# Optimization experiments

Measured on AMD Instinct MI355X. Metric: run time of the kernel, lower is better.

Reference implementation:

```python
import jax, jax.numpy as jnp
import numpy as np
from jax import lax

C = 16        # class_nums
START = 14    # tag_to_idx['<START>']
STOP = 15     # tag_to_idx['<STOP>']
NEG = -10000.0
B, T, V, E, H = 64, 512, 50000, 512, 1024
HD = H // 2   # per-direction hidden size


def setup_inputs() -> dict:
    key = jax.random.key(0)
    ks = jax.random.split(key, 16)
    s = 0.05
    inp = {}
    inp["sentence"] = jax.random.randint(ks[0], (B, T), 0, V)
    inp["embedding"] = jax.random.normal(ks[1], (V, E), jnp.float32) * 0.1
    # LSTM params, torch layout: [4*HD, Din] with gate order i,f,g,o; leading dim 2 = (fwd, bwd)
    inp["w_ih_l0"] = jax.random.normal(ks[2], (2, 4 * HD, E), jnp.float32) * s
    inp["w_hh_l0"] = jax.random.normal(ks[3], (2, 4 * HD, HD), jnp.float32) * s
    inp["b_ih_l0"] = jax.random.normal(ks[4], (2, 4 * HD), jnp.float32) * s
    inp["b_hh_l0"] = jax.random.normal(ks[5], (2, 4 * HD), jnp.float32) * s
    inp["w_ih_l1"] = jax.random.normal(ks[6], (2, 4 * HD, H), jnp.float32) * s
    inp["w_hh_l1"] = jax.random.normal(ks[7], (2, 4 * HD, HD), jnp.float32) * s
    inp["b_ih_l1"] = jax.random.normal(ks[8], (2, 4 * HD), jnp.float32) * s
    inp["b_hh_l1"] = jax.random.normal(ks[9], (2, 4 * HD), jnp.float32) * s
    inp["lin_w"] = jax.random.normal(ks[10], (C, H), jnp.float32) * s
    inp["lin_b"] = jax.random.normal(ks[11], (C,), jnp.float32) * s
    tr = jax.random.normal(ks[12], (C, C), jnp.float32)
    inp["transitions"] = tr.at[START, :].set(NEG).at[:, STOP].set(NEG)
    # init_hidden(): random (h0, c0), shape [2*num_layers, B, HD]
    inp["h0"] = jax.random.normal(ks[13], (4, B, HD), jnp.float32)
    inp["c0"] = jax.random.normal(ks[14], (4, B, HD), jnp.float32)
    return inp


def _lstm_dir(x, w_ih, w_hh, b_ih, b_hh, h0, c0, reverse):
    # x: [T, B, Din] -> hs: [T, B, HD]
    def step(carry, xt):
        h, c = carry
        g = xt @ w_ih.T + h @ w_hh.T + b_ih + b_hh  # [B, 4*HD]
        i, f, gc, o = jnp.split(g, 4, axis=-1)       # torch gate order: i, f, g, o
        c = jax.nn.sigmoid(f) * c + jax.nn.sigmoid(i) * jnp.tanh(gc)
        h = jax.nn.sigmoid(o) * jnp.tanh(c)
        return (h, c), h
    _, hs = lax.scan(step, (h0, c0), x, reverse=reverse)
    return hs


def _features(sentence, embedding, w_ih_l0, w_hh_l0, b_ih_l0, b_hh_l0,
              w_ih_l1, w_hh_l1, b_ih_l1, b_hh_l1, lin_w, lin_b, h0, c0):
    x = embedding[sentence].transpose(1, 0, 2)  # [T, B, E]
    # layer 0 (bidirectional)
    hf = _lstm_dir(x, w_ih_l0[0], w_hh_l0[0], b_ih_l0[0], b_hh_l0[0], h0[0], c0[0], False)
    hb = _lstm_dir(x, w_ih_l0[1], w_hh_l0[1], b_ih_l0[1], b_hh_l0[1], h0[1], c0[1], True)
    x = jnp.concatenate([hf, hb], axis=-1)      # [T, B, H]
    # layer 1 (bidirectional)
    hf = _lstm_dir(x, w_ih_l1[0], w_hh_l1[0], b_ih_l1[0], b_hh_l1[0], h0[2], c0[2], False)
    hb = _lstm_dir(x, w_ih_l1[1], w_hh_l1[1], b_ih_l1[1], b_hh_l1[1], h0[3], c0[3], True)
    x = jnp.concatenate([hf, hb], axis=-1)      # [T, B, H]
    feats = x @ lin_w.T + lin_b                 # [T, B, C]
    return feats.transpose(1, 0, 2)             # [B, T, C]


def _viterbi(feats, transitions):
    # feats: [T, C]. Vectorized over the tag dim; scan over time.
    init = jnp.full((C,), NEG, feats.dtype).at[START].set(0.0)

    def step(fv, feat_t):
        scores = fv[None, :] + transitions      # [next_tag, prev_tag]
        bp = jnp.argmax(scores, axis=1)
        return jnp.max(scores, axis=1) + feat_t, bp

    fv, bps = lax.scan(step, init, feats)       # bps: [T, C]
    terminal = fv + transitions[STOP]
    best = jnp.argmax(terminal)

    def back(tag, bp_t):
        return bp_t[tag], tag

    _, path = lax.scan(back, best, bps, reverse=True)  # [T]
    return terminal[best], path


def reference(sentence, embedding, w_ih_l0, w_hh_l0, b_ih_l0, b_hh_l0,
              w_ih_l1, w_hh_l1, b_ih_l1, b_hh_l1, lin_w, lin_b,
              transitions, h0, c0):
    feats = _features(sentence, embedding, w_ih_l0, w_hh_l0, b_ih_l0, b_hh_l0,
                      w_ih_l1, w_hh_l1, b_ih_l1, b_hh_l1, lin_w, lin_b, h0, c0)
    scores, paths = jax.vmap(_viterbi, in_axes=(0, None))(feats, transitions)
    return scores, paths
```

## Files before the change

### kernel.cpp

```cpp
#include <hip/hip_runtime.h>
#include <stdint.h>

constexpr int kB  = 64;
constexpr int kT  = 512;
constexpr int kHD = 512;
constexpr int kC  = 16;
constexpr int kL  = 32;
constexpr int kSTART = 14;
constexpr int kSTOP  = 15;
#define NEGV (-10000.0f)

typedef __bf16 bf16x8 __attribute__((ext_vector_type(8)));
typedef float  f32x4  __attribute__((ext_vector_type(4)));

union U16x8 { uint4 u; bf16x8 v; };

__device__ __forceinline__ unsigned short f2bf(float f) {
    union { float f; unsigned int u; } x; x.f = f;
    unsigned int u = x.u;
    u += 0x7fffu + ((u >> 16) & 1u);
    return (unsigned short)(u >> 16);
}
__device__ __forceinline__ float bf2f(unsigned int hbits) {
    union { unsigned int u; float f; } x; x.u = hbits << 16;
    return x.f;
}
__device__ __forceinline__ float fsig(float x) {
    return __builtin_amdgcn_rcpf(1.f + __expf(-x));
}
__device__ __forceinline__ float ftanh(float x) {
    float e = __expf(2.f * x);
    return 1.f - 2.f * __builtin_amdgcn_rcpf(e + 1.f);
}

typedef __attribute__((address_space(1))) const unsigned int GASU;
typedef __attribute__((address_space(3))) unsigned int LASU;
__device__ __forceinline__ void ld_lds16(const unsigned short* g, unsigned short* l) {
    __builtin_amdgcn_global_load_lds((GASU*)g, (LASU*)l, 16, 0, 0);
}

__global__ void k_castWx(const float* __restrict__ src, unsigned short* __restrict__ dst, int K) {
    int np = blockIdx.x;
    int dd = np >> 11, r = np & 2047;
    int g = r & 3, cj = r >> 2;
    const float* s = src + ((size_t)(dd * 2048 + g * 512 + cj)) * K;
    unsigned short* d = dst + (size_t)np * K;
    for (int e = threadIdx.x * 8; e < K; e += 128 * 8) {
        float4 a = *(const float4*)(s + e);
        float4 b = *(const float4*)(s + e + 4);
        ushort4 lo, hi;
        lo.x = f2bf(a.x); lo.y = f2bf(a.y); lo.z = f2bf(a.z); lo.w = f2bf(a.w);
        hi.x = f2bf(b.x); hi.y = f2bf(b.y); hi.z = f2bf(b.z); hi.w = f2bf(b.w);
        *(ushort4*)(d + e) = lo; *(ushort4*)(d + e + 4) = hi;
    }
}

__global__ void k_embed(const int* __restrict__ sent, const float* __restrict__ emb,
                        unsigned short* __restrict__ X0) {
    int row = blockIdx.x;
    int t = row >> 6, b = row & 63;
    int v = sent[b * kT + t];
    const float4* src = (const float4*)(emb + (size_t)v * 512);
    float4 f = src[threadIdx.x];
    ushort4 o;
    o.x = f2bf(f.x); o.y = f2bf(f.y); o.z = f2bf(f.z); o.w = f2bf(f.w);
    ((ushort4*)(X0 + (size_t)row * 512))[threadIdx.x] = o;
}

__global__ void k_init(const float* __restrict__ h0, const float* __restrict__ c0,
                       const float* __restrict__ bih0, const float* __restrict__ bhh0,
                       const float* __restrict__ bih1, const float* __restrict__ bhh1,
                       const float* __restrict__ lw,
                       unsigned short* __restrict__ hcur, float* __restrict__ ccur,
                       float* __restrict__ biascat0, float* __restrict__ biascat1,
                       unsigned int* __restrict__ flags, unsigned short* __restrict__ lwb) {
    int i = blockIdx.x * blockDim.x + threadIdx.x;
    const int NS = 4 * kB * kHD;
    if (i < NS) {
        int l = i >> 16;
        int rem = i & 65535;
        hcur[(size_t)l * 131072 + rem] = f2bf(h0[i]);
        ccur[i] = c0[i];
    } else if (i < NS + 8192) {
        int j2 = i - NS;
        int l = j2 >> 12;
        int n = j2 & 4095;
        int dd = n >> 11, r = n & 2047;
        int g = r >> 9, cj = r & 511;
        float v = l ? (bih1[n] + bhh1[n]) : (bih0[n] + bhh0[n]);
        int np = dd * 2048 + cj * 4 + g;
        (l ? biascat1 : biascat0)[np] = v;
    } else if (i < NS + 8192 + 2048) {
        flags[i - NS - 8192] = 0u;
    } else if (i < NS + 8192 + 2048 + 16384) {
        int idx = i - NS - 8192 - 2048;
        lwb[idx] = f2bf(lw[idx]);
    }
}

__launch_bounds__(256, 2)
__global__ void k_gemm(const unsigned short* __restrict__ A,
                       const unsigned short* __restrict__ Bm,
                       const float* __restrict__ bias,
                       unsigned short* __restrict__ Cm,
                       int K, int afwd, int abwd) {
    const int nb = blockIdx.x & 31;
    const int mb = blockIdx.x >> 5;
    const int m0w = mb << 7;
    const int arow0 = (m0w < 2048) ? (afwd + m0w) : (abwd + (m0w - 2048));
    const int n0 = nb << 7;
    const int tid = threadIdx.x;
    const int lane = tid & 63;
    const int wave = tid >> 6;
    const int wm = wave >> 1, wn = wave & 1;
    const int l16 = lane & 15, quad = lane >> 4;
    __shared__ unsigned short As[128 * 32];
    __shared__ unsigned short Bs[128 * 32];
    const int srw = wave * 32 + (lane >> 2);
    const int sc  = lane & 3;
    unsigned short* AsW0 = As + wave * 1024;
    unsigned short* AsW1 = As + wave * 1024 + 512;
    unsigned short* BsW0 = Bs + wave * 1024;
    unsigned short* BsW1 = Bs + wave * 1024 + 512;

    f32x4 acc[4][4];
    #pragma unroll
    for (int i = 0; i < 4; ++i)
        #pragma unroll
        for (int jj = 0; jj < 4; ++jj) acc[i][jj] = (f32x4){0,0,0,0};

    const int kiters = K >> 5;
    for (int kk = 0; kk < kiters; ++kk) {
        __syncthreads();
        ld_lds16(A  + (size_t)(arow0 + srw)      * K + kk * 32 + sc * 8, AsW0);
        ld_lds16(A  + (size_t)(arow0 + srw + 16) * K + kk * 32 + sc * 8, AsW1);
        ld_lds16(Bm + (size_t)(n0 + srw)         * K + kk * 32 + sc * 8, BsW0);
        ld_lds16(Bm + (size_t)(n0 + srw + 16)    * K + kk * 32 + sc * 8, BsW1);
        __syncthreads();
        U16x8 af[4], bf[4];
        #pragma unroll
        for (int i = 0; i < 4; ++i) {
            af[i].u = *(const uint4*)(As + (wm * 64 + i * 16 + l16) * 32 + quad * 8);
            bf[i].u = *(const uint4*)(Bs + (wn * 64 + i * 16 + l16) * 32 + quad * 8);
        }
        #pragma unroll
        for (int i = 0; i < 4; ++i)
            #pragma unroll
            for (int jj = 0; jj < 4; ++jj)
                acc[i][jj] = __builtin_amdgcn_mfma_f32_16x16x32_bf16(af[i].v, bf[jj].v, acc[i][jj], 0, 0, 0);
    }
    #pragma unroll
    for (int jj = 0; jj < 4; ++jj) {
        int n = n0 + wn * 64 + jj * 16 + l16;
        float bv = bias[n];
        #pragma unroll
        for (int i = 0; i < 4; ++i) {
            int mrow = m0w + wm * 64 + i * 16 + quad * 4;
            #pragma unroll
            for (int rr = 0; rr < 4; ++rr)
                Cm[(size_t)(mrow + rr) * 4096 + n] = f2bf(acc[i][jj][rr] + bv);
        }
    }
}

__launch_bounds__(512, 1)
__global__ void k_fused(const unsigned short* __restrict__ Wh,
                        const unsigned short* __restrict__ Gx,
                        unsigned short* __restrict__ hcur,
                        float* __restrict__ cc,
                        unsigned short* __restrict__ hs,
                        unsigned short* __restrict__ S,
                        unsigned int* __restrict__ flags,
                        int s0, int split,
                        const unsigned short* __restrict__ Ag,
                        const unsigned short* __restrict__ Wxg,
                        const float* __restrict__ biasg,
                        unsigned short* __restrict__ Gxout,
                        int Kg, int gfwd, int gbwd, int do_gemm) {
    __shared__ __align__(16) char smem[52928];
    const int tid = threadIdx.x;

    if (blockIdx.x < 64) {
        unsigned short* zbuf   = (unsigned short*)smem;
        float*          gsAll  = (float*)(smem + 33280);
        unsigned short* hstU16 = (unsigned short*)(smem + 50688);
        unsigned long long* hU = (unsigned long long*)(smem + 50688);
        const int blk = blockIdx.x;
        const int d  = blk >> 5;
        const int bh = (blk >> 4) & 1;
        const int wc = blk & 15;
        const int wave = tid >> 6;
        const int lane = tid & 63;
        const int l16 = lane & 15;
        const int quad = lane >> 4;
        const int r4 = lane >> 2;
        const int u  = lane & 3;
        const int col = wc * 32 + wave * 4 + u;
        float* gw = gsAll + wave * 544;

        uint4 wreg[16];
        {
            const unsigned short* wrow =
                Wh + ((size_t)d * 2048 + wc * 128 + wave * 16 + l16) * 512 + quad * 8;
            #pragma unroll
            for (int kk = 0; kk < 16; ++kk) wreg[kk] = *(const uint4*)(wrow + kk * 32);
        }
        float cst[2];
        #pragma unroll
        for (int mt = 0; mt < 2; ++mt)
            cst[mt] = cc[((size_t)d * 64 + bh * 32 + mt * 16 + r4) * 512 + col];

        unsigned int* flg = flags + (d * 2 + bh) * 256;

        for (int sl = 0; sl < kL; ++sl) {
            const int s = s0 + sl;
            const int t = d ? (kT - 1 - s) : s;
            ushort4 gx4[2];
            #pragma unroll
            for (int mt = 0; mt < 2; ++mt) {
                int b = bh * 32 + mt * 16 + r4;
                int grow = d ? (2048 + (kL - 1 - sl) * 64 + b) : (sl * 64 + b);
                gx4[mt] = *(const ushort4*)(Gx + (size_t)grow * 4096 + d * 2048 + col * 4);
            }
            if (sl > 0) {
                if (wave == 0 && lane < 16) {
                    unsigned tgt = (unsigned)s;
                    while (__hip_atomic_load(flg + lane * 16, __ATOMIC_RELAXED,
                                             __HIP_MEMORY_SCOPE_AGENT) < tgt)
                        __builtin_amdgcn_s_sleep(1);
                }
                __syncthreads();
            }
            {
                const unsigned long long* hread = (const unsigned long long*)
                    (hcur + ((size_t)((s & 1) * 2 + d) * 64 + bh * 32) * 512);
                #pragma unroll
                for (int k = 0; k < 8; ++k) {
                    int idx = tid + k * 512;
                    int r = idx >> 7, c8 = idx & 127;
                    unsigned long long v = __hip_atomic_load(hread + r * 128 + c8,
                                                             __ATOMIC_RELAXED,
                                                             __HIP_MEMORY_SCOPE_AGENT);
                    *(unsigned long long*)(zbuf + r * 520 + c8 * 4) = v;
                }
            }
            __syncthreads();
            f32x4 acc[2];
            acc[0] = (f32x4){0, 0, 0, 0};
            acc[1] = (f32x4){0, 0, 0, 0};
            #pragma unroll
            for (int kk = 0; kk < 16; ++kk) {
                U16x8 b; b.u = wreg[kk];
                #pragma unroll
                for (int mt = 0; mt < 2; ++mt) {
                    U16x8 a; a.u = *(const uint4*)(zbuf + (mt * 16 + l16) * 520 + kk * 32 + quad * 8);
                    acc[mt] = __builtin_amdgcn_mfma_f32_16x16x32_bf16(a.v, b.v, acc[mt], 0, 0, 0);
                }
            }
            #pragma unroll
            for (int mt = 0; mt < 2; ++mt)
                #pragma unroll
                for (int rr = 0; rr < 4; ++rr)
                    gw[mt * 272 + (quad * 4 + rr) * 17 + l16] = acc[mt][rr];
            asm volatile("s_waitcnt lgkmcnt(0)" ::: "memory");
            __builtin_amdgcn_sched_barrier(0);
            #pragma unroll
            for (int mt = 0; mt < 2; ++mt) {
                const float* gb = gw + mt * 272 + r4 * 17 + u * 4;
                float gi = gb[0] + bf2f(gx4[mt].x);
                float gf = gb[1] + bf2f(gx4[mt].y);
                float gg = gb[2] + bf2f(gx4[mt].z);
                float go = gb[3] + bf2f(gx4[mt].w);
                float si = fsig(gi);
                float sf = fsig(gf);
                float so = fsig(go);
                float tg = ftanh(gg);
                float cn = sf * cst[mt] + si * tg;
                cst[mt] = cn;
                float hn = so * ftanh(cn);
                hstU16[(wave * 35 + mt * 16 + r4) * 4 + u] = f2bf(hn);
            }
            __syncthreads();
            if (tid < 256) {
                int r = tid >> 3, uu = tid & 7;
                unsigned long long val = hU[uu * 35 + r];
                unsigned long long* hwrite = (unsigned long long*)
                    (hcur + ((size_t)(((s + 1) & 1) * 2 + d) * 64 + bh * 32) * 512);
                __hip_atomic_store(hwrite + r * 128 + wc * 8 + uu, val,
                                   __ATOMIC_RELAXED, __HIP_MEMORY_SCOPE_AGENT);
            }
            __syncthreads();
            if (tid == 0 && sl + 1 < kL)
                __hip_atomic_store(flg + wc * 16, (unsigned)(s + 1),
                                   __ATOMIC_RELAXED, __HIP_MEMORY_SCOPE_AGENT);
            if (tid >= 256) {
                int q = tid - 256;
                int r = q >> 3, uu = q & 7;
                unsigned long long val = hU[uu * 35 + r];
                int b = bh * 32 + r;
                bool toS = split && (d ? (t >= 256) : (t < 256));
                if (toS)
                    *(unsigned long long*)(S + ((size_t)t * 64 + b) * 512 + wc * 32 + uu * 4) = val;
                else
                    *(unsigned long long*)(hs + ((size_t)t * 64 + b) * 1024 + (size_t)d * 512 + wc * 32 + uu * 4) = val;
            }
        }
        #pragma unroll
        for (int mt = 0; mt < 2; ++mt)
            cc[((size_t)d * 64 + bh * 32 + mt * 16 + r4) * 512 + col] = cst[mt];
    } else {
        if (!do_gemm) return;
        const int gw = blockIdx.x - 64;
        const int half = tid >> 8;
        const int tid2 = tid & 255;
        const int w4 = tid2 >> 6;
        const int lane = tid2 & 63;
        const int l16 = lane & 15, quad = lane >> 4;
        unsigned short* As = (unsigned short*)(smem + half * 16384);
        unsigned short* Bs = (unsigned short*)(smem + half * 16384 + 8192);
        const int srw = w4 * 32 + (lane >> 2);
        const int sc  = lane & 3;
        const int wm = w4 >> 1, wn = w4 & 1;
        unsigned short* AsW0 = As + w4 * 1024;
        unsigned short* AsW1 = As + w4 * 1024 + 512;
        unsigned short* BsW0 = Bs + w4 * 1024;
        unsigned short* BsW1 = Bs + w4 * 1024 + 512;
        const int kiters = Kg >> 5;

        for (int pp = gw; pp < 512; pp += 192) {
            const int mb = pp >> 4;
            const int nb = ((pp & 15) << 1) + half;
            const int m0w = mb << 7;
            const int arow0 = (m0w < 2048) ? (gfwd + m0w) : (gbwd + (m0w - 2048));
            const int n0 = nb << 7;
            f32x4 acc[4][4];
            #pragma unroll
            for (int i = 0; i < 4; ++i)
                #pragma unroll
                for (int jj = 0; jj < 4; ++jj) acc[i][jj] = (f32x4){0,0,0,0};
            for (int kk = 0; kk < kiters; ++kk) {
                __syncthreads();
                ld_lds16(Ag  + (size_t)(arow0 + srw)      * Kg + kk * 32 + sc * 8, AsW0);
                ld_lds16(Ag  + (size_t)(arow0 + srw + 16) * Kg + kk * 32 + sc * 8, AsW1);
                ld_lds16(Wxg + (size_t)(n0 + srw)         * Kg + kk * 32 + sc * 8, BsW0);
                ld_lds16(Wxg + (size_t)(n0 + srw + 16)    * Kg + kk * 32 + sc * 8, BsW1);
                __syncthreads();
                U16x8 af[4], bf[4];
                #pragma unroll
                for (int i = 0; i < 4; ++i) {
                    af[i].u = *(const uint4*)(As + (wm * 64 + i * 16 + l16) * 32 + quad * 8);
                    bf[i].u = *(const uint4*)(Bs + (wn * 64 + i * 16 + l16) * 32 + quad * 8);
                }
                #pragma unroll
                for (int i = 0; i < 4; ++i)
                    #pragma unroll
                    for (int jj = 0; jj < 4; ++jj)
                        acc[i][jj] = __builtin_amdgcn_mfma_f32_16x16x32_bf16(af[i].v, bf[jj].v, acc[i][jj], 0, 0, 0);
            }
            #pragma unroll
            for (int jj = 0; jj < 4; ++jj) {
                int n = n0 + wn * 64 + jj * 16 + l16;
                float bv = biasg[n];
                #pragma unroll
                for (int i = 0; i < 4; ++i) {
                    int mrow = m0w + wm * 64 + i * 16 + quad * 4;
                    #pragma unroll
                    for (int rr = 0; rr < 4; ++rr)
                        Gxout[(size_t)(mrow + rr) * 4096 + n] = f2bf(acc[i][jj][rr] + bv);
                }
            }
        }
    }
}

__global__ void k_linear(const unsigned short* __restrict__ hs1,
                         const unsigned short* __restrict__ S,
                         const unsigned short* __restrict__ lwb,
                         const float* __restrict__ lb,
                         float* __restrict__ feats) {
    const int t = blockIdx.x;
    const int tid = threadIdx.x;
    const int wave = tid >> 6;
    const int lane = tid & 63;
    const int l16 = lane & 15, quad = lane >> 4;
    __shared__ unsigned short lws[16 * 1032];
    {
        #pragma unroll
        for (int i = 0; i < 8; ++i) {
            int idx = tid + i * 256;
            int n = idx >> 7, c = idx & 127;
            *(uint4*)(lws + n * 1032 + c * 8) = *(const uint4*)(lwb + n * 1024 + c * 8);
        }
    }
    __syncthreads();
    const int brow = wave * 16 + l16;
    f32x4 acc = {0, 0, 0, 0};
    #pragma unroll
    for (int kk = 0; kk < 32; ++kk) {
        int k0 = kk * 32 + quad * 8;
        const unsigned short* p;
        if (kk < 16)
            p = (t < 256) ? S   + ((size_t)t * 64 + brow) * 512  + k0
                          : hs1 + ((size_t)t * 64 + brow) * 1024 + k0;
        else
            p = (t >= 256) ? S   + ((size_t)t * 64 + brow) * 512  + (k0 - 512)
                           : hs1 + ((size_t)t * 64 + brow) * 1024 + k0;
        U16x8 a; a.u = *(const uint4*)p;
        U16x8 b; b.u = *(const uint4*)(lws + l16 * 1032 + k0);
        acc = __builtin_amdgcn_mfma_f32_16x16x32_bf16(a.v, b.v, acc, 0, 0, 0);
    }
    float bv = lb[l16];
    #pragma unroll
    for (int rr = 0; rr < 4; ++rr) {
        int b = wave * 16 + quad * 4 + rr;
        feats[(size_t)b * (kT * kC) + t * kC + l16] = acc[rr] + bv;
    }
}

__global__ void k_viterbi(const float* __restrict__ feats, const float* __restrict__ trans,
                          float* __restrict__ out) {
    int b = blockIdx.x;
    int lane = threadIdx.x;
    __shared__ unsigned char bp[kT * kC];
    __shared__ float fv[2][kC];
    __shared__ float tbuf[kC];
    float trow[16];
    float tstop = 0.f;
    if (lane < 16) {
        #pragma unroll
        for (int p = 0; p < 16; ++p) trow[p] = trans[lane * 16 + p];
        tstop = trans[kSTOP * 16 + lane];
        fv[0][lane] = (lane == kSTART) ? 0.f : NEGV;
    }
    __syncthreads();
    const float* fb = feats + (size_t)b * (kT * kC);
    for (int t = 0; t < kT; ++t) {
        if (lane < 16) {
            float m = -3.4e38f; int arg = 0;
            #pragma unroll
            for (int p = 0; p < 16; ++p) {
                float v = fv[t & 1][p] + trow[p];
                if (v > m) { m = v; arg = p; }
            }
            bp[t * 16 + lane] = (unsigned char)arg;
            fv[(t + 1) & 1][lane] = m + fb[t * 16 + lane];
        }
        __syncthreads();
    }
    if (lane < 16) tbuf[lane] = fv[kT & 1][lane] + tstop;
    __syncthreads();
    if (lane == 0) {
        float bm = tbuf[0]; int best = 0;
        #pragma unroll
        for (int p = 1; p < 16; ++p) if (tbuf[p] > bm) { bm = tbuf[p]; best = p; }
        out[b] = bm;
        float* path = out + kB + (size_t)b * kT;
        int tag = best;
        for (int t = kT - 1; t >= 0; --t) {
            path[t] = (float)tag;
            tag = bp[t * 16 + tag];
        }
    }
}

extern "C" void kernel_launch(void* const* d_in, const int* in_sizes, int n_in,
                              void* d_out, int out_size, void* d_ws, size_t ws_size,
                              hipStream_t stream) {
    const int*   sent = (const int*)d_in[0];
    const float* emb  = (const float*)d_in[1];
    const float* wih0 = (const float*)d_in[2];
    const float* whh0 = (const float*)d_in[3];
    const float* bih0 = (const float*)d_in[4];
    const float* bhh0 = (const float*)d_in[5];
    const float* wih1 = (const float*)d_in[6];
    const float* whh1 = (const float*)d_in[7];
    const float* bih1 = (const float*)d_in[8];
    const float* bhh1 = (const float*)d_in[9];
    const float* lw   = (const float*)d_in[10];
    const float* lb   = (const float*)d_in[11];
    const float* tr   = (const float*)d_in[12];
    const float* h0   = (const float*)d_in[13];
    const float* c0   = (const float*)d_in[14];
    float* out = (float*)d_out;

    char* ws = (char*)d_ws;
    size_t off = 0;
    auto alloc = [&](size_t bytes) -> void* {
        void* p = ws + off; off += (bytes + 255) & ~(size_t)255; return p;
    };
    unsigned short* X0    = (unsigned short*)alloc((size_t)kT * kB * 512 * 2);
    unsigned short* Wx0   = (unsigned short*)alloc((size_t)4096 * 512 * 2);
    unsigned short* S     = (unsigned short*)X0;
    unsigned short* Wh0   = (unsigned short*)alloc((size_t)4096 * 512 * 2);
    unsigned short* Wx1   = (unsigned short*)alloc((size_t)4096 * 1024 * 2);
    unsigned short* Wh1   = (unsigned short*)alloc((size_t)4096 * 512 * 2);
    float*          biascat0 = (float*)alloc(4096 * 4);
    float*          biascat1 = (float*)alloc(4096 * 4);
    unsigned short* HS    = (unsigned short*)alloc((size_t)kT * kB * 1024 * 2);
    unsigned short* hcur  = (unsigned short*)alloc((size_t)2 * 2 * 2 * kB * kHD * 2);
    float*          ccur  = (float*)alloc((size_t)4 * kB * kHD * 4);
    float*          feats = (float*)alloc((size_t)kB * kT * kC * 4);
    unsigned int*   flags = (unsigned int*)alloc(2048 * 4);
    unsigned short* lwb   = (unsigned short*)alloc(16384 * 2);
    unsigned short* Gx0   = (unsigned short*)alloc((size_t)4096 * 4096 * 2);
    unsigned short* Gx1   = (unsigned short*)alloc((size_t)4096 * 4096 * 2);
    unsigned short* GxB[2] = {Gx0, Gx1};

    k_castWx<<<4096, 128, 0, stream>>>(wih0, Wx0, 512);
    k_castWx<<<4096, 128, 0, stream>>>(whh0, Wh0, 512);
    k_castWx<<<4096, 128, 0, stream>>>(wih1, Wx1, 1024);
    k_castWx<<<4096, 128, 0, stream>>>(whh1, Wh1, 512);
    k_init<<<(4 * kB * kHD + 8192 + 2048 + 16384 + 255) / 256, 256, 0, stream>>>(
        h0, c0, bih0, bhh0, bih1, bhh1, lw, hcur, ccur, biascat0, biascat1, flags, lwb);
    k_embed<<<kT * kB, 128, 0, stream>>>(sent, emb, X0);

    unsigned short* hcur1 = hcur + (size_t)131072;
    float*          ccur1 = ccur + (size_t)65536;

    k_gemm<<<1024, 256, 0, stream>>>(X0, Wx0, biascat0, Gx0, 512, 0, (kT - kL) * 64);
    for (int ch = 0; ch < 16; ++ch) {
        int s0n = (ch + 1) * kL;
        k_fused<<<256, 512, 0, stream>>>(Wh0, GxB[ch & 1], hcur, ccur, HS, S, flags, ch * kL, 0,
                                         X0, Wx0, biascat0, GxB[(ch + 1) & 1], 512,
                                         s0n * 64, (kT - kL - s0n) * 64, ch < 15);
    }
    k_gemm<<<1024, 256, 0, stream>>>(HS, Wx1, biascat1, Gx0, 1024, 0, (kT - kL) * 64);
    for (int ch = 0; ch < 16; ++ch) {
        int s0n = (ch + 1) * kL;
        k_fused<<<256, 512, 0, stream>>>(Wh1, GxB[ch & 1], hcur1, ccur1, HS, S, flags + 1024, ch * kL, 1,
                                         HS, Wx1, biascat1, GxB[(ch + 1) & 1], 1024,
                                         s0n * 64, (kT - kL - s0n) * 64, ch < 15);
    }

    k_linear<<<kT, 256, 0, stream>>>(HS, S, lwb, lb, feats);
    k_viterbi<<<kB, 64, 0, stream>>>(feats, tr, out);
}
```

Baseline: 5.069 ms.

## Replace flag-based step barrier with sequence-tagged hidden-state words

The per-step cross-block synchronization in the recurrent LSTM kernel is changed. Each 32-bit pair of bf16 hidden values is now packed with the step number in its upper 32 bits. Consumers spin on the data words themselves until every tag reaches the current step, instead of polling separate flags and then running a block barrier. This removes the flag store/load round trip and one __syncthreads per step, so exchange latency on the serial critical path should drop. The cost is doubling the exchanged bytes and having every thread poll, which adds memory traffic and atomic loads.

```diff
diff --git a/kernel.cpp b/kernel.cpp
--- a/kernel.cpp
+++ b/kernel.cpp
@@ -38,6 +38,7 @@
 __device__ __forceinline__ void ld_lds16(const unsigned short* g, unsigned short* l) {
     __builtin_amdgcn_global_load_lds((GASU*)g, (LASU*)l, 16, 0, 0);
 }
+
 
 __global__ void k_castWx(const float* __restrict__ src, unsigned short* __restrict__ dst, int K) {
     int np = blockIdx.x;
@@ -71,15 +72,13 @@
                        const float* __restrict__ bih0, const float* __restrict__ bhh0,
                        const float* __restrict__ bih1, const float* __restrict__ bhh1,
                        const float* __restrict__ lw,
-                       unsigned short* __restrict__ hcur, float* __restrict__ ccur,
+                       unsigned long long* __restrict__ Xex, float* __restrict__ ccur,
                        float* __restrict__ biascat0, float* __restrict__ biascat1,
-                       unsigned int* __restrict__ flags, unsigned short* __restrict__ lwb) {
+                       unsigned short* __restrict__ lwb) {
     int i = blockIdx.x * blockDim.x + threadIdx.x;
     const int NS = 4 * kB * kHD;
+    const int NX = 65536;
     if (i < NS) {
-        int l = i >> 16;
-        int rem = i & 65535;
-        hcur[(size_t)l * 131072 + rem] = f2bf(h0[i]);
         ccur[i] = c0[i];
     } else if (i < NS + 8192) {
         int j2 = i - NS;
@@ -90,11 +89,22 @@
         float v = l ? (bih1[n] + bhh1[n]) : (bih0[n] + bhh0[n]);
         int np = dd * 2048 + cj * 4 + g;
         (l ? biascat1 : biascat0)[np] = v;
-    } else if (i < NS + 8192 + 2048) {
-        flags[i - NS - 8192] = 0u;
-    } else if (i < NS + 8192 + 2048 + 16384) {
-        int idx = i - NS - 8192 - 2048;
+    } else if (i < NS + 8192 + 16384) {
+        int idx = i - NS - 8192;
         lwb[idx] = f2bf(lw[idx]);
+    } else if (i < NS + 8192 + 16384 + NX) {
+        int u = i - (NS + 8192 + 16384);
+        int l = u >> 15, rem = u & 32767;
+        int d = rem >> 14, rem2 = rem & 16383;
+        int b = rem2 >> 8, q2 = rem2 & 255;
+        int j0 = q2 * 2;
+        const float* hp = h0 + ((size_t)(l * 2 + d) * 64 + b) * 512 + j0;
+        unsigned int pay = (unsigned)f2bf(hp[0]) | ((unsigned)f2bf(hp[1]) << 16);
+        Xex[(size_t)l * 65536 + ((size_t)d * 64 + b) * 256 + q2] = (unsigned long long)pay;
+    } else if (i < NS + 8192 + 16384 + 2 * NX) {
+        int u = i - (NS + 8192 + 16384 + NX);
+        int l = u >> 15, rem = u & 32767;
+        Xex[(size_t)l * 65536 + 32768 + rem] = 0ull;
     }
 }
 
@@ -166,11 +176,10 @@
 __launch_bounds__(512, 1)
 __global__ void k_fused(const unsigned short* __restrict__ Wh,
                         const unsigned short* __restrict__ Gx,
-                        unsigned short* __restrict__ hcur,
+                        unsigned long long* __restrict__ Xex,
                         float* __restrict__ cc,
                         unsigned short* __restrict__ hs,
                         unsigned short* __restrict__ S,
-                        unsigned int* __restrict__ flags,
                         int s0, int split,
                         const unsigned short* __restrict__ Ag,
                         const unsigned short* __restrict__ Wxg,
@@ -197,6 +206,7 @@
         const int u  = lane & 3;
         const int col = wc * 32 + wave * 4 + u;
         float* gw = gsAll + wave * 544;
+        const int r8 = tid >> 3, u8 = tid & 7;
 
         uint4 wreg[16];
         {
@@ -210,8 +220,6 @@
         for (int mt = 0; mt < 2; ++mt)
             cst[mt] = cc[((size_t)d * 64 + bh * 32 + mt * 16 + r4) * 512 + col];
 
-        unsigned int* flg = flags + (d * 2 + bh) * 256;
-
         for (int sl = 0; sl < kL; ++sl) {
             const int s = s0 + sl;
             const int t = d ? (kT - 1 - s) : s;
@@ -222,26 +230,43 @@
                 int grow = d ? (2048 + (kL - 1 - sl) * 64 + b) : (sl * 64 + b);
                 gx4[mt] = *(const ushort4*)(Gx + (size_t)grow * 4096 + d * 2048 + col * 4);
             }
-            if (sl > 0) {
-                if (wave == 0 && lane < 16) {
-                    unsigned tgt = (unsigned)s;
-                    while (__hip_atomic_load(flg + lane * 16, __ATOMIC_RELAXED,
-                                             __HIP_MEMORY_SCOPE_AGENT) < tgt)
-                        __builtin_amdgcn_s_sleep(1);
-                }
-                __syncthreads();
-            }
             {
-                const unsigned long long* hread = (const unsigned long long*)
-                    (hcur + ((size_t)((s & 1) * 2 + d) * 64 + bh * 32) * 512);
+                const unsigned long long* xb =
+                    Xex + ((size_t)((s & 1) * 2 + d) * 64 + bh * 32) * 256;
+                const unsigned sq = (unsigned)s;
+                unsigned long long va[8], vb[8];
                 #pragma unroll
                 for (int k = 0; k < 8; ++k) {
                     int idx = tid + k * 512;
-                    int r = idx >> 7, c8 = idx & 127;
-                    unsigned long long v = __hip_atomic_load(hread + r * 128 + c8,
-                                                             __ATOMIC_RELAXED,
-                                                             __HIP_MEMORY_SCOPE_AGENT);
-                    *(unsigned long long*)(zbuf + r * 520 + c8 * 4) = v;
+                    int r = idx >> 7, q = idx & 127;
+                    const unsigned long long* p = xb + r * 256 + q * 2;
+                    va[k] = __hip_atomic_load(p,     __ATOMIC_RELAXED, __HIP_MEMORY_SCOPE_AGENT);
+                    vb[k] = __hip_atomic_load(p + 1, __ATOMIC_RELAXED, __HIP_MEMORY_SCOPE_AGENT);
+                }
+                for (;;) {
+                    int stale = 0;
+                    #pragma unroll
+                    for (int k = 0; k < 8; ++k) {
+                        int idx = tid + k * 512;
+                        int r = idx >> 7, q = idx & 127;
+                        const unsigned long long* p = xb + r * 256 + q * 2;
+                        if ((unsigned)(va[k] >> 32) < sq) {
+                            va[k] = __hip_atomic_load(p, __ATOMIC_RELAXED, __HIP_MEMORY_SCOPE_AGENT);
+                            stale = 1;
+                        }
+                        if ((unsigned)(vb[k] >> 32) < sq) {
+                            vb[k] = __hip_atomic_load(p + 1, __ATOMIC_RELAXED, __HIP_MEMORY_SCOPE_AGENT);
+                            stale = 1;
+                        }
+                    }
+                    if (!stale) break;
+                }
+                #pragma unroll
+                for (int k = 0; k < 8; ++k) {
+                    int idx = tid + k * 512;
+                    int r = idx >> 7, q = idx & 127;
+                    unsigned long long pay = (va[k] & 0xffffffffull) | (vb[k] << 32);
+                    *(unsigned long long*)(zbuf + r * 520 + q * 4) = pay;
                 }
             }
             __syncthreads();
@@ -282,18 +307,16 @@
             }
             __syncthreads();
             if (tid < 256) {
-                int r = tid >> 3, uu = tid & 7;
-                unsigned long long val = hU[uu * 35 + r];
-                unsigned long long* hwrite = (unsigned long long*)
-                    (hcur + ((size_t)(((s + 1) & 1) * 2 + d) * 64 + bh * 32) * 512);
-                __hip_atomic_store(hwrite + r * 128 + wc * 8 + uu, val,
-                                   __ATOMIC_RELAXED, __HIP_MEMORY_SCOPE_AGENT);
-            }
-            __syncthreads();
-            if (tid == 0 && sl + 1 < kL)
-                __hip_atomic_store(flg + wc * 16, (unsigned)(s + 1),
-                                   __ATOMIC_RELAXED, __HIP_MEMORY_SCOPE_AGENT);
-            if (tid >= 256) {
+                unsigned long long hv = hU[u8 * 35 + r8];
+                unsigned long long sq1 = (unsigned long long)(unsigned)(s + 1) << 32;
+                unsigned long long A  = (hv & 0xffffffffull) | sq1;
+                unsigned long long Bv = (hv >> 32) | sq1;
+                unsigned long long* xw =
+                    Xex + ((size_t)(((s + 1) & 1) * 2 + d) * 64 + bh * 32 + r8) * 256
+                        + (wc * 8 + u8) * 2;
+                __hip_atomic_store(xw,     A,  __ATOMIC_RELAXED, __HIP_MEMORY_SCOPE_AGENT);
+                __hip_atomic_store(xw + 1, Bv, __ATOMIC_RELAXED, __HIP_MEMORY_SCOPE_AGENT);
+            } else {
                 int q = tid - 256;
                 int r = q >> 3, uu = q & 7;
                 unsigned long long val = hU[uu * 35 + r];
@@ -497,10 +520,9 @@
     float*          biascat0 = (float*)alloc(4096 * 4);
     float*          biascat1 = (float*)alloc(4096 * 4);
     unsigned short* HS    = (unsigned short*)alloc((size_t)kT * kB * 1024 * 2);
-    unsigned short* hcur  = (unsigned short*)alloc((size_t)2 * 2 * 2 * kB * kHD * 2);
+    unsigned long long* Xex = (unsigned long long*)alloc((size_t)2 * 65536 * 8);
     float*          ccur  = (float*)alloc((size_t)4 * kB * kHD * 4);
     float*          feats = (float*)alloc((size_t)kB * kT * kC * 4);
-    unsigned int*   flags = (unsigned int*)alloc(2048 * 4);
     unsigned short* lwb   = (unsigned short*)alloc(16384 * 2);
     unsigned short* Gx0   = (unsigned short*)alloc((size_t)4096 * 4096 * 2);
     unsigned short* Gx1   = (unsigned short*)alloc((size_t)4096 * 4096 * 2);
@@ -510,24 +532,24 @@
     k_castWx<<<4096, 128, 0, stream>>>(whh0, Wh0, 512);
     k_castWx<<<4096, 128, 0, stream>>>(wih1, Wx1, 1024);
     k_castWx<<<4096, 128, 0, stream>>>(whh1, Wh1, 512);
-    k_init<<<(4 * kB * kHD + 8192 + 2048 + 16384 + 255) / 256, 256, 0, stream>>>(
-        h0, c0, bih0, bhh0, bih1, bhh1, lw, hcur, ccur, biascat0, biascat1, flags, lwb);
+    k_init<<<(131072 + 8192 + 16384 + 2 * 65536) / 256, 256, 0, stream>>>(
+        h0, c0, bih0, bhh0, bih1, bhh1, lw, Xex, ccur, biascat0, biascat1, lwb);
     k_embed<<<kT * kB, 128, 0, stream>>>(sent, emb, X0);
 
-    unsigned short* hcur1 = hcur + (size_t)131072;
-    float*          ccur1 = ccur + (size_t)65536;
+    unsigned long long* Xex1 = Xex + (size_t)65536;
+    float*              ccur1 = ccur + (size_t)65536;
 
     k_gemm<<<1024, 256, 0, stream>>>(X0, Wx0, biascat0, Gx0, 512, 0, (kT - kL) * 64);
     for (int ch = 0; ch < 16; ++ch) {
         int s0n = (ch + 1) * kL;
-        k_fused<<<256, 512, 0, stream>>>(Wh0, GxB[ch & 1], hcur, ccur, HS, S, flags, ch * kL, 0,
+        k_fused<<<256, 512, 0, stream>>>(Wh0, GxB[ch & 1], Xex, ccur, HS, S, ch * kL, 0,
                                          X0, Wx0, biascat0, GxB[(ch + 1) & 1], 512,
                                          s0n * 64, (kT - kL - s0n) * 64, ch < 15);
     }
     k_gemm<<<1024, 256, 0, stream>>>(HS, Wx1, biascat1, Gx0, 1024, 0, (kT - kL) * 64);
     for (int ch = 0; ch < 16; ++ch) {
         int s0n = (ch + 1) * kL;
-        k_fused<<<256, 512, 0, stream>>>(Wh1, GxB[ch & 1], hcur1, ccur1, HS, S, flags + 1024, ch * kL, 1,
+        k_fused<<<256, 512, 0, stream>>>(Wh1, GxB[ch & 1], Xex1, ccur1, HS, S, ch * kL, 1,
                                          HS, Wx1, biascat1, GxB[(ch + 1) & 1], 1024,
                                          s0n * 64, (kT - kL - s0n) * 64, ch < 15);
     }
```

Measured after the change: 4.673 ms. 1.08x faster.
